# Optimization experiments

Measured on AMD Instinct MI355X. Metric: run time of the kernel, lower is better.

Reference implementation:

```python
import jax, jax.numpy as jnp
import numpy as np

B, S, H = 4, 4096, 1024
E, TOP_K, F = 8, 2, 4 * H  # num_experts, top_k, SwiGLU intermediate dim


def setup_inputs() -> dict:
    key = jax.random.key(0)
    k0, k1, k2, k3, k4 = jax.random.split(key, 5)
    init = 0.02  # typical transformer init scale
    return {
        "X": jax.random.normal(k0, (B, S, H), jnp.float32),
        "Wr": jax.random.normal(k1, (H, E), jnp.float32) * init,
        "W1": jax.random.normal(k2, (E, H, F), jnp.float32) * init,  # gate proj
        "W2": jax.random.normal(k3, (E, F, H), jnp.float32) * init,  # down proj
        "W3": jax.random.normal(k4, (E, H, F), jnp.float32) * init,  # up proj
    }


def reference(X, Wr, W1, W2, W3):
    bsz, seq_len, hidden = X.shape
    x = X.reshape(-1, hidden)  # [N, H]
    # Router: softmax over experts, top-k selection, renormalized weights
    router_logits = x @ Wr  # [N, E]
    probs = jax.nn.softmax(router_logits, axis=-1)
    top_w, top_i = jax.lax.top_k(probs, TOP_K)  # [N, K]
    top_w = top_w / jnp.sum(top_w, axis=-1, keepdims=True)
    # Combine: equivalent to the torch gather/index_add dispatch loop.
    # Per-expert dense SwiGLU weighted by the (possibly zero) routing weight.
    out = jnp.zeros_like(x)
    for e in range(E):
        w_e = jnp.sum(jnp.where(top_i == e, top_w, 0.0), axis=-1)  # [N]
        h = (jax.nn.silu(x @ W1[e]) * (x @ W3[e])) @ W2[e]  # [N, H]
        out = out + h * w_e[:, None]
    return out.reshape(bsz, seq_len, hidden), router_logits
```

## Files before the change

### kernel.cpp

```cpp
#include <hip/hip_runtime.h>
#include <hip/hip_bf16.h>

#define NTOK 16384
#define HD 1024
#define NE 8
#define FD 4096
#define BM 128
#define MAXTILES 264

typedef short short8 __attribute__((ext_vector_type(8)));
typedef unsigned short ushort8 __attribute__((ext_vector_type(8)));
typedef float f32x4 __attribute__((ext_vector_type(4)));

__device__ __forceinline__ unsigned short f2bf(float f) {
    unsigned int u = __builtin_bit_cast(unsigned int, f);
    u += 0x7fffu + ((u >> 16) & 1u);
    return (unsigned short)(u >> 16);
}

__device__ __forceinline__ void gld16(unsigned short* lds, const unsigned short* gp) {
    __builtin_amdgcn_global_load_lds(
        (const __attribute__((address_space(1))) unsigned int*)gp,
        (__attribute__((address_space(3))) unsigned int*)lds,
        16, 0, 0);
}

__global__ void zero16_kernel(uint4* __restrict__ p, int n16) {
    int t = blockIdx.x * 256 + threadIdx.x;
    if (t < n16) p[t] = make_uint4(0u, 0u, 0u, 0u);
}

__global__ __launch_bounds__(256)
void router_kernel(const float* __restrict__ X, const float* __restrict__ Wr,
                   float* __restrict__ logits_out, int* __restrict__ te,
                   float* __restrict__ tw) {
    int wave = threadIdx.x >> 6, lane = threadIdx.x & 63;
    int token = blockIdx.x * 4 + wave;
    const float* x = X + (size_t)token * HD;
    float acc[NE];
#pragma unroll
    for (int e = 0; e < NE; e++) acc[e] = 0.f;
#pragma unroll 4
    for (int j = 0; j < HD / 64; j++) {
        int i = lane + 64 * j;
        float xv = x[i];
        float4 w0 = *(const float4*)(Wr + (size_t)i * NE);
        float4 w1 = *(const float4*)(Wr + (size_t)i * NE + 4);
        acc[0] += xv * w0.x; acc[1] += xv * w0.y;
        acc[2] += xv * w0.z; acc[3] += xv * w0.w;
        acc[4] += xv * w1.x; acc[5] += xv * w1.y;
        acc[6] += xv * w1.z; acc[7] += xv * w1.w;
    }
#pragma unroll
    for (int off = 32; off >= 1; off >>= 1)
#pragma unroll
        for (int e = 0; e < NE; e++)
            acc[e] += __shfl_xor(acc[e], off, 64);
    if (lane < NE) logits_out[(size_t)token * NE + lane] = acc[lane];
    if (lane == 0) {
        int i1 = 0;
#pragma unroll
        for (int e = 1; e < NE; e++) if (acc[e] > acc[i1]) i1 = e;
        int i2 = (i1 == 0) ? 1 : 0;
#pragma unroll
        for (int e = 0; e < NE; e++) if (e != i1 && acc[e] > acc[i2]) i2 = e;
        float w0 = 1.f / (1.f + __expf(acc[i2] - acc[i1]));
        te[token * 2] = i1; te[token * 2 + 1] = i2;
        tw[token * 2] = w0; tw[token * 2 + 1] = 1.f - w0;
    }
}

__global__ void hist_kernel(const int* __restrict__ te, int* __restrict__ meta) {
    __shared__ int c[NE];
    int t = threadIdx.x;
    if (t < NE) c[t] = 0;
    __syncthreads();
    int tok = blockIdx.x * 256 + t;
    atomicAdd(&c[te[tok * 2]], 1);
    atomicAdd(&c[te[tok * 2 + 1]], 1);
    __syncthreads();
    if (t < NE) atomicAdd(&meta[t], c[t]);
}

__global__ void scan_kernel(int* __restrict__ meta) {
    if (threadIdx.x == 0) {
        int* counts = meta;
        int* offs   = meta + 8;
        int* tb     = meta + 17;
        int* cur    = meta + 26;
        offs[0] = 0; tb[0] = 0;
        for (int e = 0; e < NE; e++) {
            offs[e + 1] = offs[e] + counts[e];
            tb[e + 1] = tb[e] + (counts[e] + BM - 1) / BM;
            cur[e] = offs[e];
        }
    }
}

__global__ void scatter_kernel(const int* __restrict__ te, const float* __restrict__ tw,
                               int* __restrict__ meta, int* __restrict__ tok_ids,
                               float* __restrict__ aw) {
    __shared__ int c[NE];
    __shared__ int base[NE];
    int t = threadIdx.x;
    if (t < NE) c[t] = 0;
    __syncthreads();
    int tok = blockIdx.x * 256 + t;
    int e0 = te[tok * 2], e1 = te[tok * 2 + 1];
    int i0 = atomicAdd(&c[e0], 1);
    int i1 = atomicAdd(&c[e1], 1);
    __syncthreads();
    if (t < NE) base[t] = atomicAdd(&meta[26 + t], c[t]);
    __syncthreads();
    int p0 = base[e0] + i0, p1 = base[e1] + i1;
    tok_ids[p0] = tok; aw[p0] = tw[tok * 2];
    tok_ids[p1] = tok; aw[p1] = tw[tok * 2 + 1];
}

__global__ void convert_x_kernel(const float* __restrict__ in, unsigned short* __restrict__ out) {
    size_t t = (size_t)blockIdx.x * 256 + threadIdx.x;
    float4 a = ((const float4*)in)[t * 2];
    float4 b = ((const float4*)in)[t * 2 + 1];
    ushort8 o;
    o[0] = f2bf(a.x); o[1] = f2bf(a.y); o[2] = f2bf(a.z); o[3] = f2bf(a.w);
    o[4] = f2bf(b.x); o[5] = f2bf(b.y); o[6] = f2bf(b.z); o[7] = f2bf(b.w);
    *(ushort8*)(out + t * 8) = o;
}

__global__ __launch_bounds__(256)
void transpose_convert_kernel(const float* __restrict__ in, unsigned short* __restrict__ out,
                              int R, int C) {
    __shared__ float tile[64][65];
    int e = blockIdx.z;
    int c0 = blockIdx.x * 64, r0 = blockIdx.y * 64;
    const float* src = in + (size_t)e * R * C;
    unsigned short* dst = out + (size_t)e * R * C;
    int t = threadIdx.x;
#pragma unroll
    for (int i = 0; i < 4; i++) {
        int idx = t + i * 256;
        int row = idx >> 4, c4 = (idx & 15) * 4;
        float4 v = *(const float4*)(src + (size_t)(r0 + row) * C + c0 + c4);
        tile[row][c4] = v.x; tile[row][c4 + 1] = v.y;
        tile[row][c4 + 2] = v.z; tile[row][c4 + 3] = v.w;
    }
    __syncthreads();
#pragma unroll
    for (int i = 0; i < 2; i++) {
        int idx = t + i * 256;
        int c = idx >> 3, rc = (idx & 7) * 8;
        ushort8 o;
#pragma unroll
        for (int j = 0; j < 8; j++) o[j] = f2bf(tile[rc + j][c]);
        *(ushort8*)(dst + (size_t)(c0 + c) * R + r0 + rc) = o;
    }
}

__global__ __launch_bounds__(256, 2)
void moe_gemm_a(const unsigned short* __restrict__ Xb,
                const unsigned short* __restrict__ W1t,
                const unsigned short* __restrict__ W3t,
                unsigned short* __restrict__ hbuf,
                const int* __restrict__ meta,
                const int* __restrict__ tok_ids,
                int f0, int FC) {
    const int* counts = meta;
    const int* offs = meta + 8;
    const int* tb = meta + 17;
    int by = blockIdx.y;
    if (by >= tb[NE]) return;
    int e = 0;
    while (by >= tb[e + 1]) e++;
    int tIdx = by - tb[e];
    int rowsBase = offs[e] + tIdx * BM;
    int rowsInTile = counts[e] - tIdx * BM;
    if (rowsInTile > BM) rowsInTile = BM;
    int n0 = blockIdx.x * 128;

    __shared__ unsigned short As[128 * 32];
    __shared__ unsigned short B1s[128 * 32];
    __shared__ unsigned short B3s[128 * 32];

    int t = threadIdx.x;
    int wave = t >> 6, lane = t & 63, q = lane >> 4, m = lane & 15;
    int wr = (wave >> 1) * 64, wc = (wave & 1) * 64;
    int pos8 = (t & 3) * 8;
    int r0 = t >> 2;
    int rta = min(r0, rowsInTile - 1);
    int rtb = min(64 + r0, rowsInTile - 1);
    const unsigned short* apA = Xb + (size_t)tok_ids[rowsBase + rta] * HD + pos8;
    const unsigned short* apB = Xb + (size_t)tok_ids[rowsBase + rtb] * HD + pos8;
    const unsigned short* bp1a = W1t + ((size_t)e * FD + f0 + n0 + r0) * HD + pos8;
    const unsigned short* bp1b = W1t + ((size_t)e * FD + f0 + n0 + 64 + r0) * HD + pos8;
    const unsigned short* bp3a = W3t + ((size_t)e * FD + f0 + n0 + r0) * HD + pos8;
    const unsigned short* bp3b = W3t + ((size_t)e * FD + f0 + n0 + 64 + r0) * HD + pos8;
    unsigned short* dA0 = As + t * 8;
    unsigned short* dA1 = As + 2048 + t * 8;
    unsigned short* d10 = B1s + t * 8;
    unsigned short* d11 = B1s + 2048 + t * 8;
    unsigned short* d30 = B3s + t * 8;
    unsigned short* d31 = B3s + 2048 + t * 8;
    const unsigned short* raf[4];
    const unsigned short* rb1[4];
    const unsigned short* rb3[4];
#pragma unroll
    for (int ri = 0; ri < 4; ri++) raf[ri] = As + (wr + ri * 16 + m) * 32 + q * 8;
#pragma unroll
    for (int ci = 0; ci < 4; ci++) {
        rb1[ci] = B1s + (wc + ci * 16 + m) * 32 + q * 8;
        rb3[ci] = B3s + (wc + ci * 16 + m) * 32 + q * 8;
    }

    f32x4 accg[4][4], accu[4][4];
#pragma unroll
    for (int ri = 0; ri < 4; ri++)
#pragma unroll
        for (int ci = 0; ci < 4; ci++) {
            accg[ri][ci] = (f32x4){0.f, 0.f, 0.f, 0.f};
            accu[ri][ci] = (f32x4){0.f, 0.f, 0.f, 0.f};
        }

    for (int kt = 0; kt < HD; kt += 32) {
        __syncthreads();
        gld16(dA0, apA + kt);
        gld16(dA1, apB + kt);
        gld16(d10, bp1a + kt);
        gld16(d11, bp1b + kt);
        gld16(d30, bp3a + kt);
        gld16(d31, bp3b + kt);
        __syncthreads();
        short8 af[4], b1f[4], b3f[4];
#pragma unroll
        for (int ri = 0; ri < 4; ri++) af[ri] = *(const short8*)raf[ri];
#pragma unroll
        for (int ci = 0; ci < 4; ci++) {
            b1f[ci] = *(const short8*)rb1[ci];
            b3f[ci] = *(const short8*)rb3[ci];
        }
#pragma unroll
        for (int ri = 0; ri < 4; ri++)
#pragma unroll
            for (int ci = 0; ci < 4; ci++) {
                accg[ri][ci] = __builtin_amdgcn_mfma_f32_16x16x32_bf16(af[ri], b1f[ci], accg[ri][ci], 0, 0, 0);
                accu[ri][ci] = __builtin_amdgcn_mfma_f32_16x16x32_bf16(af[ri], b3f[ci], accu[ri][ci], 0, 0, 0);
            }
    }
#pragma unroll
    for (int ri = 0; ri < 4; ri++)
#pragma unroll
        for (int ci = 0; ci < 4; ci++)
#pragma unroll
            for (int r = 0; r < 4; r++) {
                int rl = wr + ri * 16 + q * 4 + r;
                if (rl < rowsInTile) {
                    float g = accg[ri][ci][r], u = accu[ri][ci][r];
                    float hv = g * u / (1.f + __expf(-g));
                    hbuf[(size_t)(rowsBase + rl) * FC + n0 + wc + ci * 16 + m] = f2bf(hv);
                }
            }
}

__global__ __launch_bounds__(256, 2)
void moe_gemm_b(const unsigned short* __restrict__ hbuf,
                const unsigned short* __restrict__ W2t,
                float* __restrict__ out,
                const int* __restrict__ meta,
                const int* __restrict__ tok_ids,
                const float* __restrict__ aw,
                int f0, int FC) {
    const int* counts = meta;
    const int* offs = meta + 8;
    const int* tb = meta + 17;
    int by = blockIdx.y;
    if (by >= tb[NE]) return;
    int e = 0;
    while (by >= tb[e + 1]) e++;
    int tIdx = by - tb[e];
    int rowsBase = offs[e] + tIdx * BM;
    int rowsInTile = counts[e] - tIdx * BM;
    if (rowsInTile > BM) rowsInTile = BM;
    int n0 = blockIdx.x * 128;

    __shared__ unsigned short As[128 * 32];
    __shared__ unsigned short Bs[128 * 32];

    int t = threadIdx.x;
    int wave = t >> 6, lane = t & 63, q = lane >> 4, m = lane & 15;
    int wr = (wave >> 1) * 64, wc = (wave & 1) * 64;
    int pos8 = (t & 3) * 8;
    int r0 = t >> 2;
    int rta = min(r0, rowsInTile - 1);
    int rtb = min(64 + r0, rowsInTile - 1);
    const unsigned short* apA = hbuf + (size_t)(rowsBase + rta) * FC + pos8;
    const unsigned short* apB = hbuf + (size_t)(rowsBase + rtb) * FC + pos8;
    const unsigned short* bpA = W2t + ((size_t)e * HD + n0 + r0) * FD + f0 + pos8;
    const unsigned short* bpB = W2t + ((size_t)e * HD + n0 + 64 + r0) * FD + f0 + pos8;
    unsigned short* dA0 = As + t * 8;
    unsigned short* dA1 = As + 2048 + t * 8;
    unsigned short* dB0 = Bs + t * 8;
    unsigned short* dB1 = Bs + 2048 + t * 8;
    const unsigned short* raf[4];
    const unsigned short* rbf[4];
#pragma unroll
    for (int ri = 0; ri < 4; ri++) raf[ri] = As + (wr + ri * 16 + m) * 32 + q * 8;
#pragma unroll
    for (int ci = 0; ci < 4; ci++) rbf[ci] = Bs + (wc + ci * 16 + m) * 32 + q * 8;

    f32x4 acc[4][4];
#pragma unroll
    for (int ri = 0; ri < 4; ri++)
#pragma unroll
        for (int ci = 0; ci < 4; ci++) acc[ri][ci] = (f32x4){0.f, 0.f, 0.f, 0.f};

    for (int kt = 0; kt < FC; kt += 32) {
        __syncthreads();
        gld16(dA0, apA + kt);
        gld16(dA1, apB + kt);
        gld16(dB0, bpA + kt);
        gld16(dB1, bpB + kt);
        __syncthreads();
        short8 af[4], bf[4];
#pragma unroll
        for (int ri = 0; ri < 4; ri++) af[ri] = *(const short8*)raf[ri];
#pragma unroll
        for (int ci = 0; ci < 4; ci++) bf[ci] = *(const short8*)rbf[ci];
#pragma unroll
        for (int ri = 0; ri < 4; ri++)
#pragma unroll
            for (int ci = 0; ci < 4; ci++)
                acc[ri][ci] = __builtin_amdgcn_mfma_f32_16x16x32_bf16(af[ri], bf[ci], acc[ri][ci], 0, 0, 0);
    }
#pragma unroll
    for (int ri = 0; ri < 4; ri++)
#pragma unroll
        for (int ci = 0; ci < 4; ci++)
#pragma unroll
            for (int r = 0; r < 4; r++) {
                int rl = wr + ri * 16 + q * 4 + r;
                if (rl < rowsInTile) {
                    int arow = rowsBase + rl;
                    int tok = tok_ids[arow];
                    float w = aw[arow];
                    atomicAdd(out + (size_t)tok * HD + n0 + wc + ci * 16 + m,
                              acc[ri][ci][r] * w);
                }
            }
}

extern "C" void kernel_launch(void* const* d_in, const int* in_sizes, int n_in,
                              void* d_out, int out_size, void* d_ws, size_t ws_size,
                              hipStream_t stream) {
    const float* X  = (const float*)d_in[0];
    const float* Wr = (const float*)d_in[1];
    const float* W1 = (const float*)d_in[2];
    const float* W2 = (const float*)d_in[3];
    const float* W3 = (const float*)d_in[4];
    float* out = (float*)d_out;
    float* logits_out = out + (size_t)NTOK * HD;

    char* ws = (char*)d_ws;
    size_t off = 0;
    auto alloc = [&](size_t bytes) -> void* {
        void* p = ws + off;
        off = (off + bytes + 255) & ~(size_t)255;
        return p;
    };
    unsigned short* Xb  = (unsigned short*)alloc((size_t)NTOK * HD * 2);
    unsigned short* W1t = (unsigned short*)alloc((size_t)NE * HD * FD * 2);
    unsigned short* W3t = (unsigned short*)alloc((size_t)NE * HD * FD * 2);
    unsigned short* W2t = (unsigned short*)alloc((size_t)NE * HD * FD * 2);
    int*   tok_ids = (int*)alloc((size_t)NTOK * 2 * 4);
    float* awf     = (float*)alloc((size_t)NTOK * 2 * 4);
    int*   te      = (int*)alloc((size_t)NTOK * 2 * 4);
    float* twf     = (float*)alloc((size_t)NTOK * 2 * 4);
    int*   meta    = (int*)alloc(64 * 4);
    size_t remain = ws_size > off ? ws_size - off : 0;
    int NC = 1;
    while ((size_t)NTOK * 2 * (size_t)(FD / NC) * 2 > remain && NC < 32) NC *= 2;
    int FC = FD / NC;
    unsigned short* hbuf = (unsigned short*)(ws + off);

    zero16_kernel<<<(NTOK * HD * 4 / 16 + 255) / 256, 256, 0, stream>>>((uint4*)out, NTOK * HD * 4 / 16);
    zero16_kernel<<<1, 256, 0, stream>>>((uint4*)meta, 16);

    router_kernel<<<NTOK / 4, 256, 0, stream>>>(X, Wr, logits_out, te, twf);
    hist_kernel<<<NTOK / 256, 256, 0, stream>>>(te, meta);
    scan_kernel<<<1, 64, 0, stream>>>(meta);
    scatter_kernel<<<NTOK / 256, 256, 0, stream>>>(te, twf, meta, tok_ids, awf);

    convert_x_kernel<<<NTOK * HD / 8 / 256, 256, 0, stream>>>(X, Xb);
    transpose_convert_kernel<<<dim3(FD / 64, HD / 64, NE), 256, 0, stream>>>(W1, W1t, HD, FD);
    transpose_convert_kernel<<<dim3(FD / 64, HD / 64, NE), 256, 0, stream>>>(W3, W3t, HD, FD);
    transpose_convert_kernel<<<dim3(HD / 64, FD / 64, NE), 256, 0, stream>>>(W2, W2t, FD, HD);

    for (int c = 0; c < NC; c++) {
        moe_gemm_a<<<dim3(FC / 128, MAXTILES), 256, 0, stream>>>(Xb, W1t, W3t, hbuf, meta, tok_ids, c * FC, FC);
        moe_gemm_b<<<dim3(HD / 128, MAXTILES), 256, 0, stream>>>(hbuf, W2t, out, meta, tok_ids, awf, c * FC, FC);
    }
}
```

Measured before the change: 1.699 ms.

## Double-buffer LDS tiles with XOR swizzle in both MoE GEMM kernels

Both grouped GEMM kernels now keep two LDS buffers and issue the global-to-LDS loads for the next K slice before the MFMA work on the current one, so memory latency overlaps compute and one barrier per step is dropped. Row chunks are XOR-swizzled on store and on read to avoid LDS bank conflicts. The down-projection kernel also widens its K tile from 32 to 64. LDS use per block doubles (up to 64 KB in gemm_b), which may limit occupancy, and the loop assumes FC is a multiple of 128.

```diff
diff --git a/kernel.cpp b/kernel.cpp
--- a/kernel.cpp
+++ b/kernel.cpp
@@ -156,6 +156,7 @@
     }
 }
 
+#define TA (128 * 32)
 __global__ __launch_bounds__(256, 2)
 void moe_gemm_a(const unsigned short* __restrict__ Xb,
                 const unsigned short* __restrict__ W1t,
@@ -177,39 +178,25 @@
     if (rowsInTile > BM) rowsInTile = BM;
     int n0 = blockIdx.x * 128;
 
-    __shared__ unsigned short As[128 * 32];
-    __shared__ unsigned short B1s[128 * 32];
-    __shared__ unsigned short B3s[128 * 32];
+    __shared__ unsigned short As[2 * TA];
+    __shared__ unsigned short B1s[2 * TA];
+    __shared__ unsigned short B3s[2 * TA];
 
     int t = threadIdx.x;
     int wave = t >> 6, lane = t & 63, q = lane >> 4, m = lane & 15;
     int wr = (wave >> 1) * 64, wc = (wave & 1) * 64;
-    int pos8 = (t & 3) * 8;
     int r0 = t >> 2;
+    int chk = t & 3;
+    int pos8s = (chk ^ ((r0 >> 1) & 3)) * 8;
     int rta = min(r0, rowsInTile - 1);
     int rtb = min(64 + r0, rowsInTile - 1);
-    const unsigned short* apA = Xb + (size_t)tok_ids[rowsBase + rta] * HD + pos8;
-    const unsigned short* apB = Xb + (size_t)tok_ids[rowsBase + rtb] * HD + pos8;
-    const unsigned short* bp1a = W1t + ((size_t)e * FD + f0 + n0 + r0) * HD + pos8;
-    const unsigned short* bp1b = W1t + ((size_t)e * FD + f0 + n0 + 64 + r0) * HD + pos8;
-    const unsigned short* bp3a = W3t + ((size_t)e * FD + f0 + n0 + r0) * HD + pos8;
-    const unsigned short* bp3b = W3t + ((size_t)e * FD + f0 + n0 + 64 + r0) * HD + pos8;
-    unsigned short* dA0 = As + t * 8;
-    unsigned short* dA1 = As + 2048 + t * 8;
-    unsigned short* d10 = B1s + t * 8;
-    unsigned short* d11 = B1s + 2048 + t * 8;
-    unsigned short* d30 = B3s + t * 8;
-    unsigned short* d31 = B3s + 2048 + t * 8;
-    const unsigned short* raf[4];
-    const unsigned short* rb1[4];
-    const unsigned short* rb3[4];
-#pragma unroll
-    for (int ri = 0; ri < 4; ri++) raf[ri] = As + (wr + ri * 16 + m) * 32 + q * 8;
-#pragma unroll
-    for (int ci = 0; ci < 4; ci++) {
-        rb1[ci] = B1s + (wc + ci * 16 + m) * 32 + q * 8;
-        rb3[ci] = B3s + (wc + ci * 16 + m) * 32 + q * 8;
-    }
+    const unsigned short* apA = Xb + (size_t)tok_ids[rowsBase + rta] * HD + pos8s;
+    const unsigned short* apB = Xb + (size_t)tok_ids[rowsBase + rtb] * HD + pos8s;
+    const unsigned short* bp1a = W1t + ((size_t)e * FD + f0 + n0 + r0) * HD + pos8s;
+    const unsigned short* bp1b = W1t + ((size_t)e * FD + f0 + n0 + 64 + r0) * HD + pos8s;
+    const unsigned short* bp3a = W3t + ((size_t)e * FD + f0 + n0 + r0) * HD + pos8s;
+    const unsigned short* bp3b = W3t + ((size_t)e * FD + f0 + n0 + 64 + r0) * HD + pos8s;
+    int qs = (q ^ ((m >> 1) & 3)) * 8;
 
     f32x4 accg[4][4], accu[4][4];
 #pragma unroll
@@ -220,22 +207,29 @@
             accu[ri][ci] = (f32x4){0.f, 0.f, 0.f, 0.f};
         }
 
-    for (int kt = 0; kt < HD; kt += 32) {
-        __syncthreads();
-        gld16(dA0, apA + kt);
-        gld16(dA1, apB + kt);
-        gld16(d10, bp1a + kt);
-        gld16(d11, bp1b + kt);
-        gld16(d30, bp3a + kt);
-        gld16(d31, bp3b + kt);
-        __syncthreads();
+    auto stage = [&](int buf, int kt) {
+        unsigned short* a = As + buf * TA;
+        unsigned short* b1 = B1s + buf * TA;
+        unsigned short* b3 = B3s + buf * TA;
+        gld16(a + t * 8, apA + kt);
+        gld16(a + 2048 + t * 8, apB + kt);
+        gld16(b1 + t * 8, bp1a + kt);
+        gld16(b1 + 2048 + t * 8, bp1b + kt);
+        gld16(b3 + t * 8, bp3a + kt);
+        gld16(b3 + 2048 + t * 8, bp3b + kt);
+    };
+    auto compute = [&](int buf) {
+        const unsigned short* a = As + buf * TA;
+        const unsigned short* b1 = B1s + buf * TA;
+        const unsigned short* b3 = B3s + buf * TA;
         short8 af[4], b1f[4], b3f[4];
 #pragma unroll
-        for (int ri = 0; ri < 4; ri++) af[ri] = *(const short8*)raf[ri];
+        for (int ri = 0; ri < 4; ri++)
+            af[ri] = *(const short8*)(a + (wr + ri * 16 + m) * 32 + qs);
 #pragma unroll
         for (int ci = 0; ci < 4; ci++) {
-            b1f[ci] = *(const short8*)rb1[ci];
-            b3f[ci] = *(const short8*)rb3[ci];
+            b1f[ci] = *(const short8*)(b1 + (wc + ci * 16 + m) * 32 + qs);
+            b3f[ci] = *(const short8*)(b3 + (wc + ci * 16 + m) * 32 + qs);
         }
 #pragma unroll
         for (int ri = 0; ri < 4; ri++)
@@ -244,7 +238,19 @@
                 accg[ri][ci] = __builtin_amdgcn_mfma_f32_16x16x32_bf16(af[ri], b1f[ci], accg[ri][ci], 0, 0, 0);
                 accu[ri][ci] = __builtin_amdgcn_mfma_f32_16x16x32_bf16(af[ri], b3f[ci], accu[ri][ci], 0, 0, 0);
             }
-    }
+    };
+
+    stage(0, 0);
+    __syncthreads();
+    for (int kt = 0; kt < HD; kt += 64) {
+        stage(1, kt + 32);
+        compute(0);
+        __syncthreads();
+        if (kt + 64 < HD) stage(0, kt + 64);
+        compute(1);
+        __syncthreads();
+    }
+
 #pragma unroll
     for (int ri = 0; ri < 4; ri++)
 #pragma unroll
@@ -260,6 +266,7 @@
             }
 }
 
+#define TBB (128 * 64)
 __global__ __launch_bounds__(256, 2)
 void moe_gemm_b(const unsigned short* __restrict__ hbuf,
                 const unsigned short* __restrict__ W2t,
@@ -281,30 +288,25 @@
     if (rowsInTile > BM) rowsInTile = BM;
     int n0 = blockIdx.x * 128;
 
-    __shared__ unsigned short As[128 * 32];
-    __shared__ unsigned short Bs[128 * 32];
+    __shared__ unsigned short As[2 * TBB];
+    __shared__ unsigned short Bs[2 * TBB];
 
     int t = threadIdx.x;
     int wave = t >> 6, lane = t & 63, q = lane >> 4, m = lane & 15;
     int wr = (wave >> 1) * 64, wc = (wave & 1) * 64;
-    int pos8 = (t & 3) * 8;
-    int r0 = t >> 2;
-    int rta = min(r0, rowsInTile - 1);
-    int rtb = min(64 + r0, rowsInTile - 1);
-    const unsigned short* apA = hbuf + (size_t)(rowsBase + rta) * FC + pos8;
-    const unsigned short* apB = hbuf + (size_t)(rowsBase + rtb) * FC + pos8;
-    const unsigned short* bpA = W2t + ((size_t)e * HD + n0 + r0) * FD + f0 + pos8;
-    const unsigned short* bpB = W2t + ((size_t)e * HD + n0 + 64 + r0) * FD + f0 + pos8;
-    unsigned short* dA0 = As + t * 8;
-    unsigned short* dA1 = As + 2048 + t * 8;
-    unsigned short* dB0 = Bs + t * 8;
-    unsigned short* dB1 = Bs + 2048 + t * 8;
-    const unsigned short* raf[4];
-    const unsigned short* rbf[4];
-#pragma unroll
-    for (int ri = 0; ri < 4; ri++) raf[ri] = As + (wr + ri * 16 + m) * 32 + q * 8;
-#pragma unroll
-    for (int ci = 0; ci < 4; ci++) rbf[ci] = Bs + (wc + ci * 16 + m) * 32 + q * 8;
+    int r0 = t >> 3;
+    int chk = t & 7;
+    int pos8s = (chk ^ (r0 & 7)) * 8;
+    const unsigned short* apc[4];
+    const unsigned short* bpc[4];
+#pragma unroll
+    for (int c = 0; c < 4; c++) {
+        int ar = min(32 * c + r0, rowsInTile - 1);
+        apc[c] = hbuf + (size_t)(rowsBase + ar) * FC + pos8s;
+        bpc[c] = W2t + ((size_t)e * HD + n0 + 32 * c + r0) * FD + f0 + pos8s;
+    }
+    int g0 = ((q) ^ (m & 7)) * 8;
+    int g1 = ((4 + q) ^ (m & 7)) * 8;
 
     f32x4 acc[4][4];
 #pragma unroll
@@ -312,24 +314,49 @@
 #pragma unroll
         for (int ci = 0; ci < 4; ci++) acc[ri][ci] = (f32x4){0.f, 0.f, 0.f, 0.f};
 
-    for (int kt = 0; kt < FC; kt += 32) {
+    auto stage = [&](int buf, int kt) {
+        unsigned short* a = As + buf * TBB;
+        unsigned short* b = Bs + buf * TBB;
+#pragma unroll
+        for (int c = 0; c < 4; c++) {
+            gld16(a + c * 2048 + t * 8, apc[c] + kt);
+            gld16(b + c * 2048 + t * 8, bpc[c] + kt);
+        }
+    };
+    auto compute = [&](int buf) {
+        const unsigned short* a = As + buf * TBB;
+        const unsigned short* b = Bs + buf * TBB;
+        short8 af0[4], bf0[4], af1[4], bf1[4];
+#pragma unroll
+        for (int ri = 0; ri < 4; ri++) {
+            af0[ri] = *(const short8*)(a + (wr + ri * 16 + m) * 64 + g0);
+            af1[ri] = *(const short8*)(a + (wr + ri * 16 + m) * 64 + g1);
+        }
+#pragma unroll
+        for (int ci = 0; ci < 4; ci++) {
+            bf0[ci] = *(const short8*)(b + (wc + ci * 16 + m) * 64 + g0);
+            bf1[ci] = *(const short8*)(b + (wc + ci * 16 + m) * 64 + g1);
+        }
+#pragma unroll
+        for (int ri = 0; ri < 4; ri++)
+#pragma unroll
+            for (int ci = 0; ci < 4; ci++) {
+                acc[ri][ci] = __builtin_amdgcn_mfma_f32_16x16x32_bf16(af0[ri], bf0[ci], acc[ri][ci], 0, 0, 0);
+                acc[ri][ci] = __builtin_amdgcn_mfma_f32_16x16x32_bf16(af1[ri], bf1[ci], acc[ri][ci], 0, 0, 0);
+            }
+    };
+
+    stage(0, 0);
+    __syncthreads();
+    for (int kt = 0; kt < FC; kt += 128) {
+        stage(1, kt + 64);
+        compute(0);
         __syncthreads();
-        gld16(dA0, apA + kt);
-        gld16(dA1, apB + kt);
-        gld16(dB0, bpA + kt);
-        gld16(dB1, bpB + kt);
+        if (kt + 128 < FC) stage(0, kt + 128);
+        compute(1);
         __syncthreads();
-        short8 af[4], bf[4];
-#pragma unroll
-        for (int ri = 0; ri < 4; ri++) af[ri] = *(const short8*)raf[ri];
-#pragma unroll
-        for (int ci = 0; ci < 4; ci++) bf[ci] = *(const short8*)rbf[ci];
-#pragma unroll
-        for (int ri = 0; ri < 4; ri++)
-#pragma unroll
-            for (int ci = 0; ci < 4; ci++)
-                acc[ri][ci] = __builtin_amdgcn_mfma_f32_16x16x32_bf16(af[ri], bf[ci], acc[ri][ci], 0, 0, 0);
-    }
+    }
+
 #pragma unroll
     for (int ri = 0; ri < 4; ri++)
 #pragma unroll
```

After: 1.775 ms. 4.4% more time.
